# Kernel tuning notes

Measured on AMD Instinct MI355X. Metric: run time of the kernel, lower is better.

## Reference

```python
import jax, jax.numpy as jnp
import numpy as np

H = 121
W = 121
N_INTERP = 200
XRANGE0 = -15.0
YRANGE0 = -15.0
XYSTEP = 0.25
RET_PER_DVA = 280.0  # Curcio linear retinotopy, um per deg
XLOW = XRANGE0 * RET_PER_DVA   # -4200 um
XHIGH = -XLOW
YLOW = YRANGE0 * RET_PER_DVA
YHIGH = -YLOW
STEP_X = (XHIGH - XLOW) / (N_INTERP - 1)
STEP_Y = (YHIGH - YLOW) / (N_INTERP - 1)
OD_OFF_X = 15.5 * RET_PER_DVA  # optic disc location in retinal um
OD_OFF_Y = 1.5 * RET_PER_DVA
AMP_CUTOFF = 0.25
PI = np.pi
TEMP1 = 4.0 * PI  # -2*pi*log(exp(-2)) = 4*pi


def setup_inputs() -> dict:
    key = jax.random.key(0)
    ks = jax.random.split(key, 6)
    B, E = 8, 225
    # stimulus: freq (Hz), amp (xTh), pulse duration (ms)
    freq = jax.random.uniform(ks[0], (B, E)) * 20.0
    amp = jax.random.uniform(ks[1], (B, E)) * 2.0
    pdur = jax.random.uniform(ks[2], (B, E)) * 0.4 + 0.05
    stim = jnp.stack([freq, amp, pdur], axis=-1).astype(jnp.float32)
    # patient params: rho, lam, orient_scale, a0..a4, implant_x/y, rot, loc_od_x/y
    u = jax.random.uniform(ks[3], (B, 13))
    lo = jnp.array([100.0, 0.1, 0.8, 0.5, 0.3, 0.01, 0.5, -0.5, -500.0, -500.0, -0.3, OD_OFF_X - 100.0, OD_OFF_Y - 100.0])
    hi = jnp.array([400.0, 0.9, 1.2, 1.5, 0.7, 0.10, 1.5, 0.5, 500.0, 500.0, 0.3, OD_OFF_X + 100.0, OD_OFF_Y + 100.0])
    params = (lo + u * (hi - lo)).astype(jnp.float32)
    # 15x15 electrode grid, 300 um pitch, centered
    coords = (jnp.arange(15, dtype=jnp.float32) - 7.0) * 300.0
    gx, gy = jnp.meshgrid(coords, coords)
    elec_x = gx.reshape(1, -1)
    elec_y = gy.reshape(1, -1)
    # precomputed axon bundle tangent slopes on n_interp x n_interp grid, [y, x]
    slopes = jax.random.uniform(ks[4], (N_INTERP, N_INTERP), minval=-PI / 2, maxval=PI / 2).astype(jnp.float32)
    # pixelgrid exactly as in source: swapaxes(indices(shape),0,2).reshape(-1,2)
    pixelgrid = jnp.asarray(np.swapaxes(np.indices((H, W)), 0, 2).reshape(-1, 2), dtype=jnp.float32)
    return dict(stim=stim, params=params, elec_x=elec_x, elec_y=elec_y, slopes=slopes, pixelgrid=pixelgrid)


def _interp_bilinear(grid, qx, qy):
    # grid: [Ny, Nx] indexed [y, x]; matches tfa interpolate_bilinear(indexing='xy')
    ny, nx = grid.shape
    fx = jnp.clip(jnp.floor(qx), 0.0, nx - 2)
    fy = jnp.clip(jnp.floor(qy), 0.0, ny - 2)
    ix = fx.astype(jnp.int32)
    iy = fy.astype(jnp.int32)
    ax = jnp.clip(qx - fx, 0.0, 1.0)
    ay = jnp.clip(qy - fy, 0.0, 1.0)
    g00 = grid[iy, ix]
    g01 = grid[iy, ix + 1]
    g10 = grid[iy + 1, ix]
    g11 = grid[iy + 1, ix + 1]
    top = g00 + ax * (g01 - g00)
    bot = g10 + ax * (g11 - g10)
    return top + ay * (bot - top)


def reference(stim, params, elec_x, elec_y, slopes, pixelgrid):
    freq, amp, pdur = stim[..., 0], stim[..., 1], stim[..., 2]  # [B, E]
    rho = params[:, 0:1]
    lam = params[:, 1:2]
    orient_scale = params[:, 2:3]
    a0, a1, a2, a3, a4 = (params[:, i:i + 1] for i in range(3, 8))
    implant_x = params[:, 8:9]
    implant_y = params[:, 9:10]
    rot = params[:, 10:11]
    loc_od_x = params[:, 11:12]
    # rotate + translate electrodes (retinal um), [B, E]
    cr, sr = jnp.cos(rot), jnp.sin(rot)
    ex = elec_x * cr - elec_y * sr + implant_x
    ey = elec_x * sr + elec_y * cr + implant_y
    offx = loc_od_x - OD_OFF_X
    # bilinear interp of axon tangents at shifted electrode positions
    qx = (ex - offx - XLOW) / STEP_X
    qy = (ey - YLOW) / STEP_Y
    thetas = _interp_bilinear(slopes, qx, qy)
    thetas = jnp.where(thetas < -PI / 2, thetas + PI, thetas) * orient_scale
    # per electrode-phosphene MVG params
    rho_scaled = jnp.maximum(rho * amp * a3, 1.0)
    lam_scaled = jnp.clip(lam * 0.45 ** (-a4) * pdur ** a4, 0.0, 0.99)
    bright = jnp.where(amp > AMP_CUTOFF, a0 * jnp.maximum(amp, 1e-5) ** a1 + a2 * freq, 0.0)
    temp2 = jnp.sqrt(1.0 - lam_scaled ** 2)
    sy = rho_scaled / (TEMP1 * temp2)
    sx = rho_scaled * temp2 / TEMP1
    s, c = jnp.sin(thetas), jnp.cos(thetas)
    # cov = R diag(sx, sy) R^T, expanded analytically (symmetric 2x2)
    cov00 = sx * c * c + sy * s * s
    cov01 = (sx - sy) * s * c
    cov11 = sx * s * s + sy * c * c
    det = cov00 * cov11 - cov01 * cov01
    inv00 = cov11 / det
    inv01 = -cov01 / det
    inv11 = cov00 / det
    # electrode centers in pixel coords
    center_x = (ex / RET_PER_DVA - XRANGE0) / XYSTEP
    center_y = H - (ey / RET_PER_DVA - YRANGE0) / XYSTEP
    # quadratic form over all pixels: [P, B, E]
    d0 = pixelgrid[:, None, None, 0] - center_x[None]
    d1 = pixelgrid[:, None, None, 1] - center_y[None]
    t3 = d0 * d0 * inv00[None] + 2.0 * d0 * d1 * inv01[None] + d1 * d1 * inv11[None]
    imgs = jnp.sum(jnp.exp(-0.5 * t3) * bright[None], axis=-1)  # [P, B]
    img = imgs.T.reshape(-1, H, W)  # matches tf transpose+reshape
    return jnp.flip(img, axis=1)    # tf.image.flip_up_down
```

## Files before the change

kernel.cpp:

```cpp
#include <hip/hip_runtime.h>
#include <math.h>

#define Hh 121
#define Ww 121
#define NPI 200
#define Bb 8
#define Ee 225
#define NPIX (Hh * Ww)
#define TS 16
#define XT 8
#define YT 8
#define MAXC 232

#define XLOWc   (-4200.0f)
#define RSTEP   (199.0f / 8400.0f)
#define ODXc     4340.0f
#define PIc      3.14159265358979323846f
#define INV2PI   0.15915494309189535f
#define INV4PI   0.07957747154594767f
#define NHL     (-0.72134752044448170368f)
#define CULL_T   20.0f
#define NL2_045  1.15200309344504995f

#if __has_builtin(__builtin_amdgcn_exp2f)
#define EXP2F(x) __builtin_amdgcn_exp2f(x)
#else
#define EXP2F(x) exp2f(x)
#endif
#if __has_builtin(__builtin_amdgcn_logf)
#define LOG2F(x) __builtin_amdgcn_logf(x)
#else
#define LOG2F(x) log2f(x)
#endif
#if __has_builtin(__builtin_amdgcn_sinf)
#define SINR(x) __builtin_amdgcn_sinf((x) * INV2PI)
#define COSR(x) __builtin_amdgcn_cosf((x) * INV2PI)
#else
#define SINR(x) sinf(x)
#define COSR(x) cosf(x)
#endif
#if __has_builtin(__builtin_amdgcn_rcpf)
#define RCPF(x) __builtin_amdgcn_rcpf(x)
#else
#define RCPF(x) (1.0f / (x))
#endif

extern "C" __global__ void __launch_bounds__(256)
mvg_fused(const float* __restrict__ stim, const float* __restrict__ params,
          const float* __restrict__ elec_x, const float* __restrict__ elec_y,
          const float* __restrict__ slopes, float* __restrict__ out)
{
    __shared__ __align__(16) float4 scA[MAXC];
    __shared__ __align__(8)  float2 scB[MAXC];
    __shared__ int scnt;

    const int b    = blockIdx.z;
    const int tid  = threadIdx.x;
    const int lane = tid & 63;

    if (tid == 0) scnt = 0;
    __syncthreads();

    const int   jmin = blockIdx.x * TS;
    const int   jmax = min(jmin + TS - 1, Ww - 1);
    const int   imin = blockIdx.y * TS;
    const int   imax = min(imin + TS - 1, Hh - 1);
    const float pxminf = (float)jmin, pxmaxf = (float)jmax;
    const float pyminf = (float)(Hh - 1 - imax), pymaxf = (float)(Hh - 1 - imin);

    float cx = 0.f, cy = 0.f, A = 0.f, B = 0.f, C = 0.f, bright = 0.f, R = -1e9f;
    const bool has = tid < Ee;
    if (has) {
        const float* p = params + b * 13;
        const float rho = p[0], lam = p[1], osc = p[2];
        const float pa0 = p[3], pa1 = p[4], pa2 = p[5], pa3 = p[6], pa4 = p[7];
        const float impx = p[8], impy = p[9], rot = p[10], locx = p[11];

        const float cr = COSR(rot), sr = SINR(rot);
        const float exl = elec_x[tid], eyl = elec_y[tid];
        const float exv = exl * cr - eyl * sr + impx;
        const float eyv = exl * sr + eyl * cr + impy;

        const float offx = locx - ODXc;
        const float qx = (exv - offx - XLOWc) * RSTEP;
        const float qy = (eyv - XLOWc) * RSTEP;
        const float fx = fminf(fmaxf(floorf(qx), 0.0f), (float)(NPI - 2));
        const float fy = fminf(fmaxf(floorf(qy), 0.0f), (float)(NPI - 2));
        const int ix = (int)fx, iy = (int)fy;
        const float ax = fminf(fmaxf(qx - fx, 0.0f), 1.0f);
        const float ay = fminf(fmaxf(qy - fy, 0.0f), 1.0f);
        const float g00 = slopes[iy * NPI + ix];
        const float g01 = slopes[iy * NPI + ix + 1];
        const float g10 = slopes[(iy + 1) * NPI + ix];
        const float g11 = slopes[(iy + 1) * NPI + ix + 1];
        const float top = g00 + ax * (g01 - g00);
        const float bot = g10 + ax * (g11 - g10);
        float th = top + ay * (bot - top);
        th = (th < -0.5f * PIc) ? th + PIc : th;
        th *= osc;

        const float* st = stim + (b * Ee + tid) * 3;
        const float freq = st[0], amp = st[1], pdur = st[2];

        const float rho_s = fmaxf(rho * amp * pa3, 1.0f);
        float lam_s = lam * EXP2F(pa4 * (LOG2F(pdur) + NL2_045));
        lam_s = fminf(fmaxf(lam_s, 0.0f), 0.99f);
        bright = (amp > 0.25f)
                   ? (pa0 * EXP2F(pa1 * LOG2F(fmaxf(amp, 1e-5f))) + pa2 * freq)
                   : 0.0f;

        const float temp2 = sqrtf(1.0f - lam_s * lam_s);
        const float sy_ = rho_s * INV4PI * RCPF(temp2);
        const float sx_ = rho_s * temp2 * INV4PI;
        const float s = SINR(th), c = COSR(th);
        const float cov00 = sx_ * c * c + sy_ * s * s;
        const float cov01 = (sx_ - sy_) * s * c;
        const float cov11 = sx_ * s * s + sy_ * c * c;
        const float det  = cov00 * cov11 - cov01 * cov01;
        const float rdet = RCPF(det);
        const float i00 =  cov11 * rdet;
        const float i01 = -cov01 * rdet;
        const float i11 =  cov00 * rdet;

        cx = exv * (1.0f / 70.0f) + 60.0f;
        cy = 61.0f - eyv * (1.0f / 70.0f);

        A = i00 * NHL;
        B = i01 * 2.0f * NHL;
        C = i11 * NHL;

        const float a = -A, bq = -B, cc = -C;
        const float lam_min = 0.5f * ((a + cc) - sqrtf((a - cc) * (a - cc) + bq * bq));
        if (bright != 0.0f && lam_min > 0.0f)      R = sqrtf(CULL_T / lam_min) + 0.5f;
        else if (bright != 0.0f)                   R = 1e9f;
    }

    const bool live = has &&
        (cx + R >= pxminf) && (cx - R <= pxmaxf) &&
        (cy + R >= pyminf) && (cy - R <= pymaxf);

    {
        const unsigned long long m = __ballot(live);
        const int pre   = (int)__popcll(m & ((1ull << lane) - 1ull));
        const int wvcnt = (int)__popcll(m);
        int b0 = 0;
        if (lane == 0 && wvcnt) b0 = atomicAdd(&scnt, wvcnt);
        const int base = __shfl(b0, 0);
        if (live) {
            const int pos = base + pre;
            scA[pos] = make_float4(cx, cy, A, B);
            scB[pos] = make_float2(C, bright);
        }
    }
    __syncthreads();

    const int cnt = scnt;
    if (tid < 4) {
        scA[cnt + tid] = make_float4(0.f, 0.f, 0.f, 0.f);
        scB[cnt + tid] = make_float2(0.f, 0.f);
    }
    __syncthreads();
    const int n = (cnt + 3) & ~3;

    const int lx = tid & (TS - 1);
    const int ly = tid >> 4;
    const int j  = jmin + lx;
    const int i  = imin + ly;
    const float px = (float)j;
    const float py = (float)(Hh - 1 - i);

    float ac0 = 0.f, ac1 = 0.f, ac2 = 0.f, ac3 = 0.f;

#define BODY(k, acc) {                                          \
        const float4 v = scA[e + (k)];                          \
        const float2 w = scB[e + (k)];                          \
        const float dx = px - v.x;                              \
        const float dy = py - v.y;                              \
        const float u_ = fmaf(dx, v.z, dy * v.w);               \
        const float t_ = fmaf(dy * dy, w.x, dx * u_);           \
        acc = fmaf(w.y, EXP2F(t_), acc);                        \
    }

    #pragma unroll 1
    for (int e = 0; e < n; e += 4) {
        BODY(0, ac0)
        BODY(1, ac1)
        BODY(2, ac2)
        BODY(3, ac3)
    }
#undef BODY

    if (i < Hh && j < Ww)
        out[b * NPIX + i * Ww + j] = (ac0 + ac1) + (ac2 + ac3);
}

extern "C" void kernel_launch(void* const* d_in, const int* in_sizes, int n_in,
                              void* d_out, int out_size, void* d_ws, size_t ws_size,
                              hipStream_t stream) {
    const float* stim   = (const float*)d_in[0];
    const float* params = (const float*)d_in[1];
    const float* ex     = (const float*)d_in[2];
    const float* ey     = (const float*)d_in[3];
    const float* slopes = (const float*)d_in[4];
    float* out = (float*)d_out;

    dim3 grid(XT, YT, Bb);
    mvg_fused<<<grid, 256, 0, stream>>>(stim, params, ex, ey, slopes, out);
}
```

Measured before the change: 73.25 us.

## Split per-electrode setup into a precompute kernel and render with 8x8 single-wave tiles

Per-electrode Gaussian parameters were previously recomputed by every 16x16 tile block. They are now computed once per batch in a small precompute kernel and written to workspace. A render kernel with 64-thread 8x8 tiles then culls electrodes against its tile using wave ballots, with no shared atomics, and evaluates the pixels. Smaller tiles give more blocks and tighter culling, at the cost of a second launch and a global round-trip for the electrode records.

```diff
diff --git a/kernel.cpp b/kernel.cpp
--- a/kernel.cpp
+++ b/kernel.cpp
@@ -6,10 +6,9 @@
 #define NPI 200
 #define Bb 8
 #define Ee 225
+#define EPAD 256
 #define NPIX (Hh * Ww)
-#define TS 16
-#define XT 8
-#define YT 8
+#define TS 8
 #define MAXC 232
 
 #define XLOWc   (-4200.0f)
@@ -45,39 +44,27 @@
 #define RCPF(x) (1.0f / (x))
 #endif
 
-extern "C" __global__ void __launch_bounds__(256)
-mvg_fused(const float* __restrict__ stim, const float* __restrict__ params,
-          const float* __restrict__ elec_x, const float* __restrict__ elec_y,
-          const float* __restrict__ slopes, float* __restrict__ out)
+
+extern "C" __global__ void __launch_bounds__(64)
+mvg_precomp(const float* __restrict__ stim, const float* __restrict__ params,
+            const float* __restrict__ elec_x, const float* __restrict__ elec_y,
+            const float* __restrict__ slopes,
+            float4* __restrict__ cullRec, float4* __restrict__ mARec,
+            float2* __restrict__ mBRec)
 {
-    __shared__ __align__(16) float4 scA[MAXC];
-    __shared__ __align__(8)  float2 scB[MAXC];
-    __shared__ int scnt;
-
-    const int b    = blockIdx.z;
-    const int tid  = threadIdx.x;
-    const int lane = tid & 63;
-
-    if (tid == 0) scnt = 0;
-    __syncthreads();
-
-    const int   jmin = blockIdx.x * TS;
-    const int   jmax = min(jmin + TS - 1, Ww - 1);
-    const int   imin = blockIdx.y * TS;
-    const int   imax = min(imin + TS - 1, Hh - 1);
-    const float pxminf = (float)jmin, pxmaxf = (float)jmax;
-    const float pyminf = (float)(Hh - 1 - imax), pymaxf = (float)(Hh - 1 - imin);
-
-    float cx = 0.f, cy = 0.f, A = 0.f, B = 0.f, C = 0.f, bright = 0.f, R = -1e9f;
-    const bool has = tid < Ee;
-    if (has) {
+    const int b = blockIdx.x;
+    const int e = blockIdx.y * 64 + threadIdx.x;
+
+    float cx = 0.f, cy = 0.f, A = 0.f, Bq = 0.f, C = 0.f, bright = 0.f, R = -1e9f;
+
+    if (e < Ee) {
         const float* p = params + b * 13;
         const float rho = p[0], lam = p[1], osc = p[2];
         const float pa0 = p[3], pa1 = p[4], pa2 = p[5], pa3 = p[6], pa4 = p[7];
         const float impx = p[8], impy = p[9], rot = p[10], locx = p[11];
 
         const float cr = COSR(rot), sr = SINR(rot);
-        const float exl = elec_x[tid], eyl = elec_y[tid];
+        const float exl = elec_x[e], eyl = elec_y[e];
         const float exv = exl * cr - eyl * sr + impx;
         const float eyv = exl * sr + eyl * cr + impy;
 
@@ -99,7 +86,7 @@
         th = (th < -0.5f * PIc) ? th + PIc : th;
         th *= osc;
 
-        const float* st = stim + (b * Ee + tid) * 3;
+        const float* st = stim + (b * Ee + e) * 3;
         const float freq = st[0], amp = st[1], pdur = st[2];
 
         const float rho_s = fmaxf(rho * amp * pa3, 1.0f);
@@ -125,45 +112,73 @@
         cx = exv * (1.0f / 70.0f) + 60.0f;
         cy = 61.0f - eyv * (1.0f / 70.0f);
 
-        A = i00 * NHL;
-        B = i01 * 2.0f * NHL;
-        C = i11 * NHL;
-
-        const float a = -A, bq = -B, cc = -C;
+        A  = i00 * NHL;
+        Bq = i01 * 2.0f * NHL;
+        C  = i11 * NHL;
+
+        const float a = -A, bq = -Bq, cc = -C;
         const float lam_min = 0.5f * ((a + cc) - sqrtf((a - cc) * (a - cc) + bq * bq));
         if (bright != 0.0f && lam_min > 0.0f)      R = sqrtf(CULL_T / lam_min) + 0.5f;
         else if (bright != 0.0f)                   R = 1e9f;
     }
 
-    const bool live = has &&
-        (cx + R >= pxminf) && (cx - R <= pxmaxf) &&
-        (cy + R >= pyminf) && (cy - R <= pymaxf);
-
-    {
-        const unsigned long long m = __ballot(live);
-        const int pre   = (int)__popcll(m & ((1ull << lane) - 1ull));
-        const int wvcnt = (int)__popcll(m);
-        int b0 = 0;
-        if (lane == 0 && wvcnt) b0 = atomicAdd(&scnt, wvcnt);
-        const int base = __shfl(b0, 0);
-        if (live) {
-            const int pos = base + pre;
-            scA[pos] = make_float4(cx, cy, A, B);
-            scB[pos] = make_float2(C, bright);
-        }
-    }
-    __syncthreads();
-
-    const int cnt = scnt;
-    if (tid < 4) {
-        scA[cnt + tid] = make_float4(0.f, 0.f, 0.f, 0.f);
-        scB[cnt + tid] = make_float2(0.f, 0.f);
+    const int idx = b * EPAD + e;
+    cullRec[idx] = make_float4(cx, cy, R, 0.f);
+    mARec[idx]   = make_float4(cx, cy, A, Bq);
+    mBRec[idx]   = make_float2(C, bright);
+}
+
+extern "C" __global__ void __launch_bounds__(64)
+mvg_render(const float4* __restrict__ cullRec, const float4* __restrict__ mARec,
+           const float2* __restrict__ mBRec, float* __restrict__ out)
+{
+    __shared__ __align__(16) float4 scA[MAXC];
+    __shared__ __align__(8)  float2 scB[MAXC];
+
+    const int b    = blockIdx.z;
+    const int lane = threadIdx.x;
+
+    const int   jmin = blockIdx.x * TS;
+    const int   imin = blockIdx.y * TS;
+    const int   jmax = min(jmin + TS - 1, Ww - 1);
+    const int   imax = min(imin + TS - 1, Hh - 1);
+    const float pxminf = (float)jmin, pxmaxf = (float)jmax;
+    const float pyminf = (float)(Hh - 1 - imax), pymaxf = (float)(Hh - 1 - imin);
+
+    const int base = b * EPAD + lane;
+    const float4 c0 = cullRec[base      ], c1 = cullRec[base +  64],
+                 c2 = cullRec[base + 128], c3 = cullRec[base + 192];
+    const float4 a0 = mARec[base      ], a1 = mARec[base +  64],
+                 a2 = mARec[base + 128], a3 = mARec[base + 192];
+    const float2 b0 = mBRec[base      ], b1 = mBRec[base +  64],
+                 b2 = mBRec[base + 128], b3 = mBRec[base + 192];
+
+    int cnt = 0;
+#define CHUNK(cv, av, bv) {                                                    \
+        const bool live = (cv.x + cv.z >= pxminf) && (cv.x - cv.z <= pxmaxf) && \
+                          (cv.y + cv.z >= pyminf) && (cv.y - cv.z <= pymaxf);   \
+        const unsigned long long m = __ballot(live);                            \
+        if (live) {                                                             \
+            const int pos = cnt + (int)__popcll(m & ((1ull << lane) - 1ull));   \
+            scA[pos] = av; scB[pos] = bv;                                       \
+        }                                                                       \
+        cnt += (int)__popcll(m);                                                \
+    }
+    CHUNK(c0, a0, b0)
+    CHUNK(c1, a1, b1)
+    CHUNK(c2, a2, b2)
+    CHUNK(c3, a3, b3)
+#undef CHUNK
+
+    if (lane < 4) {
+        scA[cnt + lane] = make_float4(0.f, 0.f, 0.f, 0.f);
+        scB[cnt + lane] = make_float2(0.f, 0.f);
     }
     __syncthreads();
     const int n = (cnt + 3) & ~3;
 
-    const int lx = tid & (TS - 1);
-    const int ly = tid >> 4;
+    const int lx = lane & (TS - 1);
+    const int ly = lane >> 3;
     const int j  = jmin + lx;
     const int i  = imin + ly;
     const float px = (float)j;
@@ -204,6 +219,11 @@
     const float* slopes = (const float*)d_in[4];
     float* out = (float*)d_out;
 
-    dim3 grid(XT, YT, Bb);
-    mvg_fused<<<grid, 256, 0, stream>>>(stim, params, ex, ey, slopes, out);
+    float4* cullRec = (float4*)d_ws;
+    float4* mARec   = cullRec + Bb * EPAD;
+    float2* mBRec   = (float2*)(mARec + Bb * EPAD);
+
+    mvg_precomp<<<dim3(Bb, 4), 64, 0, stream>>>(stim, params, ex, ey, slopes,
+                                                cullRec, mARec, mBRec);
+    mvg_render<<<dim3(16, 16, Bb), 64, 0, stream>>>(cullRec, mARec, mBRec, out);
 }
```

Result: no change. 74.37 us (+1.5%).
